# Kernel optimization log

Hardware: AMD Instinct MI355X
Metric: run time of the kernel (lower is better)

The kernel has to match this reference:

```python
import jax, jax.numpy as jnp
import numpy as np

WIN = 256  # window_size from init_kwargs


def _stream_attn(q, k, v, win, hollow):
    """Banded sliding-window attention.

    hollow=False (s-stream): key j attended iff 0 <= i - j < win (last `win` tokens incl. self).
    hollow=True  (c-stream): key j attended iff win <= i - j < 2*win (tokens [i-2W+1, i-W]).
    Returns (out [B,S,H,D], lse [B,H,S]) with lse = -inf for fully-masked rows.
    """
    B, S, H, D = q.shape
    nb = S // win
    scale = D ** -0.5
    qb = q.reshape(B, nb, win, H, D)
    kb = k.reshape(B, nb, win, H, D)
    vb = v.reshape(B, nb, win, H, D)
    pad = ((0, 0), (2, 0), (0, 0), (0, 0), (0, 0))
    kp = jnp.pad(kb, pad)
    vp = jnp.pad(vb, pad)
    k_ctx = jnp.concatenate([kp[:, t:t + nb] for t in range(3)], axis=2)  # [B,nb,3W,H,D]
    v_ctx = jnp.concatenate([vp[:, t:t + nb] for t in range(3)], axis=2)
    lq = jnp.arange(win)[:, None]
    kk = jnp.arange(3 * win)[None, :]
    t_blk = kk // win
    lk = kk % win
    rel = (2 - t_blk) * win + lq - lk  # i - j, shape [W, 3W]
    if hollow:
        wmask = (rel >= win) & (rel < 2 * win)
    else:
        wmask = (rel >= 0) & (rel < win)
    blk_ok = (jnp.arange(nb)[:, None] - 2 + (jnp.arange(3 * win) // win)[None, :]) >= 0  # [nb,3W]
    mask = wmask[None] & blk_ok[:, None, :]  # [nb, W, 3W]
    logits = jnp.einsum('bnqhd,bnkhd->bnhqk', qb, k_ctx) * scale  # [B,nb,H,W,3W]
    logits = jnp.where(mask[None, :, None], logits, -jnp.inf)
    m = jnp.max(logits, axis=-1)  # [B,nb,H,W]
    ms = jnp.where(jnp.isneginf(m), 0.0, m)
    p = jnp.exp(logits - ms[..., None])
    denom = jnp.sum(p, axis=-1)  # [B,nb,H,W]
    out = jnp.einsum('bnhqk,bnkhd->bnqhd', p, v_ctx)  # [B,nb,W,H,D]
    safe = jnp.where(denom > 0, denom, 1.0)
    out = out / jnp.moveaxis(safe, 2, 3)[..., None]
    lse = jnp.where(denom > 0, jnp.log(safe) + m, -jnp.inf)  # [B,nb,H,W]
    out = out.reshape(B, S, H, D)
    lse = jnp.moveaxis(lse, 1, 2).reshape(B, H, S)
    return out, lse


def _merge(out_c, lse_c, out_s, lse_s):
    # faithful jax version of merge_attn_states_torch (LSE online-softmax merge)
    m = jnp.maximum(lse_c, lse_s)
    ms = jnp.where(jnp.isneginf(m), 0.0, m)
    ec = jnp.exp(lse_c - ms)
    es = jnp.exp(lse_s - ms)
    se = ec + es  # s-stream always has >=1 key (self), so se > 0
    c_scale = jnp.moveaxis(ec / se, 1, 2)[..., None]  # [B,S,H,1]
    s_scale = jnp.moveaxis(es / se, 1, 2)[..., None]
    return out_c * c_scale + out_s * s_scale


def setup_inputs() -> dict:
    key = jax.random.key(0)
    k1, k2, k3 = jax.random.split(key, 3)
    B, S, H, D = 2, 2048, 16, 128
    return {
        'query': jax.random.normal(k1, (B, S, H, D), dtype=jnp.float32),
        'key': jax.random.normal(k2, (B, S, H, D), dtype=jnp.float32),
        'value': jax.random.normal(k3, (B, S, H, D), dtype=jnp.float32),
    }


def reference(query, key, value):
    out_c, lse_c = _stream_attn(query, key, value, WIN, hollow=True)   # c-stream: [i-2W, i-W]
    out_s, lse_s = _stream_attn(query, key, value, WIN, hollow=False)  # s-stream: last W tokens
    return _merge(out_c, lse_c, out_s, lse_s)
```

## Files before the change

kernel.cpp:

```cpp
#include <hip/hip_runtime.h>
#include <math.h>

#define S_LEN 2048
#define NH    16
#define DD    128
#define SROW  (NH*DD)
#define WIN2  512
#define BQ    128
#define BK    64
#define RSQ   136
#define RS    72

typedef __bf16 bf16x8 __attribute__((ext_vector_type(8)));
typedef __bf16 bf16x4 __attribute__((ext_vector_type(4)));
typedef float  f32x4  __attribute__((ext_vector_type(4)));

__device__ __forceinline__ f32x4 mfma16(bf16x8 a, bf16x8 b, f32x4 c) {
    return __builtin_amdgcn_mfma_f32_16x16x32_bf16(a, b, c, 0, 0, 0);
}

__device__ __forceinline__ unsigned int pack_bf16(float lo, float hi) {
    return (unsigned int)__builtin_bit_cast(unsigned short, (__bf16)lo)
         | ((unsigned int)__builtin_bit_cast(unsigned short, (__bf16)hi) << 16);
}

#define OFF_VT 8704
#define OFF_P  17920
#define SMEM_ELEMS 27136

__global__ __launch_bounds__(256, 2)
void swattn_kernel(const float* __restrict__ Qg, const float* __restrict__ Kg,
                   const float* __restrict__ Vg, float* __restrict__ Og) {
    __shared__ __align__(16) __bf16 smem[SMEM_ELEMS];

    const int t   = threadIdx.x;
    const int w   = t >> 6;
    const int l   = t & 63;
    const int r16 = l & 15;
    const int g4  = l >> 4;
    const int qt  = blockIdx.x;
    const int h   = blockIdx.y;
    const int b   = blockIdx.z;
    const int Qlo = qt * BQ;

    const size_t bh = ((size_t)b * S_LEN) * SROW + (size_t)h * DD;

    for (int it = 0; it < 16; ++it) {
        int f   = it * 256 + t;
        int q_l = f >> 5;
        int dq  = (f & 31) * 4;
        const float4 v = *(const float4*)&Qg[bh + (size_t)(Qlo + q_l) * SROW + dq];
        bf16x4 o4 = { (__bf16)v.x, (__bf16)v.y, (__bf16)v.z, (__bf16)v.w };
        *(bf16x4*)&smem[q_l * RSQ + dq] = o4;
    }
    __syncthreads();

    bf16x8 qf[2][4];
#pragma unroll
    for (int qg = 0; qg < 2; ++qg)
#pragma unroll
        for (int sl = 0; sl < 4; ++sl)
            qf[qg][sl] = *(const bf16x8*)&smem[(w*32 + qg*16 + r16) * RSQ + sl*32 + g4*8];
    __syncthreads();

    const f32x4 zero4 = {0.f, 0.f, 0.f, 0.f};
    f32x4 oacc[8][2];
#pragma unroll
    for (int dg = 0; dg < 8; ++dg) { oacc[dg][0] = zero4; oacc[dg][1] = zero4; }
    float m_run[2] = { -1e30f, -1e30f };
    float l_run[2] = { 0.f, 0.f };

    const int q_lo_w = Qlo + w * 32;
    const int q_hi_w = q_lo_w + 31;
    const float C1 = 0.08838834764831845f * 1.44269504088896340f;

    int cb = Qlo - (WIN2 - 1);
    if (cb < 0) cb = 0;
    cb &= ~(BK - 1);
    const int Qhi = Qlo + BQ - 1;

    for (int c0 = cb; c0 <= Qhi; c0 += BK) {
        for (int it = 0; it < 8; ++it) {
            int f   = it * 256 + t;
            int k_l = f >> 5;
            int dq  = (f & 31) * 4;
            const float4 v = *(const float4*)&Kg[bh + (size_t)(c0 + k_l) * SROW + dq];
            bf16x4 o4 = { (__bf16)v.x, (__bf16)v.y, (__bf16)v.z, (__bf16)v.w };
            *(bf16x4*)&smem[k_l * RSQ + dq] = o4;
        }
        {
            const int gv = l >> 5;
            const int rv = l & 31;
            for (int it = 0; it < 8; ++it) {
                int k0l = w * 16 + it * 2;
                const float4 v4 = *(const float4*)&Vg[bh + (size_t)(c0 + k0l + gv) * SROW + 4*rv];
                float ox = __shfl_xor(v4.x, 32);
                float oy = __shfl_xor(v4.y, 32);
                float oz = __shfl_xor(v4.z, 32);
                float ow = __shfl_xor(v4.w, 32);
                float lo0, hi0, lo1, hi1; int d0;
                if (gv == 0) { lo0 = v4.x; hi0 = ox;   lo1 = v4.y; hi1 = oy;   d0 = 4*rv; }
                else         { lo0 = oz;   hi0 = v4.z; lo1 = ow;   hi1 = v4.w; d0 = 4*rv + 2; }
                *(unsigned int*)&smem[OFF_VT + (d0    ) * RS + k0l] = pack_bf16(lo0, hi0);
                *(unsigned int*)&smem[OFF_VT + (d0 + 1) * RS + k0l] = pack_bf16(lo1, hi1);
            }
        }
        __syncthreads();

        const bool act = (q_hi_w >= c0) && (q_lo_w <= c0 + (BK - 1) + (WIN2 - 1));
        if (act) {
            f32x4 st[4][2];
#pragma unroll
            for (int kg = 0; kg < 4; ++kg) { st[kg][0] = zero4; st[kg][1] = zero4; }
#pragma unroll
            for (int sl = 0; sl < 4; ++sl)
#pragma unroll
                for (int kg = 0; kg < 4; ++kg) {
                    bf16x8 kf = *(const bf16x8*)&smem[(kg*16 + r16) * RSQ + sl*32 + g4*8];
                    st[kg][0] = mfma16(kf, qf[0][sl], st[kg][0]);
                    st[kg][1] = mfma16(kf, qf[1][sl], st[kg][1]);
                }

            const bool fv = (q_lo_w >= c0 + (BK - 1)) && (q_hi_w <= c0 + (WIN2 - 1));
            if (fv) {
#pragma unroll
                for (int kg = 0; kg < 4; ++kg)
#pragma unroll
                    for (int qg = 0; qg < 2; ++qg)
#pragma unroll
                        for (int rg = 0; rg < 4; ++rg) st[kg][qg][rg] *= C1;
            } else {
#pragma unroll
                for (int qg = 0; qg < 2; ++qg) {
                    int iq = q_lo_w + qg*16 + r16;
#pragma unroll
                    for (int kg = 0; kg < 4; ++kg) {
                        int relb = iq - (c0 + kg*16 + 4*g4);
#pragma unroll
                        for (int rg = 0; rg < 4; ++rg) {
                            bool ok = ((unsigned)(relb - rg)) < (unsigned)WIN2;
                            st[kg][qg][rg] = ok ? st[kg][qg][rg] * C1 : -1e30f;
                        }
                    }
                }
            }

            float alpha[2];
#pragma unroll
            for (int qg = 0; qg < 2; ++qg) {
                float mc = -1e30f;
#pragma unroll
                for (int kg = 0; kg < 4; ++kg)
#pragma unroll
                    for (int rg = 0; rg < 4; ++rg) mc = fmaxf(mc, st[kg][qg][rg]);
                mc = fmaxf(mc, __shfl_xor(mc, 16));
                mc = fmaxf(mc, __shfl_xor(mc, 32));
                float mn = fmaxf(m_run[qg], mc);
                alpha[qg] = exp2f(m_run[qg] - mn);
                m_run[qg] = mn;
                float sum = 0.f;
#pragma unroll
                for (int kg = 0; kg < 4; ++kg)
#pragma unroll
                    for (int rg = 0; rg < 4; ++rg) {
                        float tv = st[kg][qg][rg];
                        float p  = exp2f(tv - mn);
                        if (!fv) p = (tv > -1e29f) ? p : 0.f;
                        st[kg][qg][rg] = p;
                        sum += p;
                    }
                sum += __shfl_xor(sum, 16);
                sum += __shfl_xor(sum, 32);
                l_run[qg] = l_run[qg] * alpha[qg] + sum;
            }

#pragma unroll
            for (int qg = 0; qg < 2; ++qg)
#pragma unroll
                for (int kg = 0; kg < 4; ++kg) {
                    f32x4 pv = st[kg][qg];
                    bf16x4 p4 = { (__bf16)pv[0], (__bf16)pv[1], (__bf16)pv[2], (__bf16)pv[3] };
                    *(bf16x4*)&smem[OFF_P + (w*32 + qg*16 + r16) * RS + kg*16 + 4*g4] = p4;
                }

#pragma unroll
            for (int dg = 0; dg < 8; ++dg)
#pragma unroll
                for (int qg = 0; qg < 2; ++qg)
#pragma unroll
                    for (int rg = 0; rg < 4; ++rg) oacc[dg][qg][rg] *= alpha[qg];

#pragma unroll
            for (int ks = 0; ks < 2; ++ks) {
                bf16x8 pf0 = *(const bf16x8*)&smem[OFF_P + (w*32 +  0 + r16) * RS + ks*32 + g4*8];
                bf16x8 pf1 = *(const bf16x8*)&smem[OFF_P + (w*32 + 16 + r16) * RS + ks*32 + g4*8];
#pragma unroll
                for (int dg = 0; dg < 8; ++dg) {
                    bf16x8 vf = *(const bf16x8*)&smem[OFF_VT + (dg*16 + r16) * RS + ks*32 + g4*8];
                    oacc[dg][0] = mfma16(vf, pf0, oacc[dg][0]);
                    oacc[dg][1] = mfma16(vf, pf1, oacc[dg][1]);
                }
            }
        }
        __syncthreads();
    }

    float inv0 = 1.f / l_run[0];
    float inv1 = 1.f / l_run[1];
#pragma unroll
    for (int qg = 0; qg < 2; ++qg) {
        float iv = qg ? inv1 : inv0;
        int q = q_lo_w + qg*16 + r16;
        size_t base = bh + (size_t)q * SROW;
#pragma unroll
        for (int dg = 0; dg < 8; ++dg) {
            f32x4 o = oacc[dg][qg];
            float4 res = { o[0]*iv, o[1]*iv, o[2]*iv, o[3]*iv };
            *(float4*)&Og[base + dg*16 + 4*g4] = res;
        }
    }
}

extern "C" void kernel_launch(void* const* d_in, const int* in_sizes, int n_in,
                              void* d_out, int out_size, void* d_ws, size_t ws_size,
                              hipStream_t stream) {
    const float* q = (const float*)d_in[0];
    const float* k = (const float*)d_in[1];
    const float* v = (const float*)d_in[2];
    float* o = (float*)d_out;
    int B = in_sizes[0] / (S_LEN * NH * DD);
    dim3 grid(S_LEN / BQ, NH, B);
    swattn_kernel<<<grid, 256, 0, stream>>>(q, k, v, o);
}
```

Before: 179.4 us.

## Shrink P buffer, raise occupancy, swizzle V^T, remap blocks per XCD, prescale Q

```diff
diff --git a/kernel.cpp b/kernel.cpp
--- a/kernel.cpp
+++ b/kernel.cpp
@@ -10,6 +10,7 @@
 #define BK    64
 #define RSQ   136
 #define RS    72
+#define RSP   40
 
 typedef __bf16 bf16x8 __attribute__((ext_vector_type(8)));
 typedef __bf16 bf16x4 __attribute__((ext_vector_type(4)));
@@ -26,9 +27,9 @@
 
 #define OFF_VT 8704
 #define OFF_P  17920
-#define SMEM_ELEMS 27136
-
-__global__ __launch_bounds__(256, 2)
+#define SMEM_ELEMS 23040
+
+__global__ __launch_bounds__(256, 3)
 void swattn_kernel(const float* __restrict__ Qg, const float* __restrict__ Kg,
                    const float* __restrict__ Vg, float* __restrict__ Og) {
     __shared__ __align__(16) __bf16 smem[SMEM_ELEMS];
@@ -38,19 +39,33 @@
     const int l   = t & 63;
     const int r16 = l & 15;
     const int g4  = l >> 4;
-    const int qt  = blockIdx.x;
-    const int h   = blockIdx.y;
-    const int b   = blockIdx.z;
+
+    int qt, h, b;
+    if (gridDim.x == 512) {
+        int xcd = blockIdx.x & 7;
+        int j   = blockIdx.x >> 3;
+        qt      = j & 15;
+        int col = xcd * 4 + (j >> 4);
+        h       = col & 15;
+        b       = col >> 4;
+    } else {
+        qt = blockIdx.x % (S_LEN / BQ);
+        int col = blockIdx.x / (S_LEN / BQ);
+        h = col % NH;
+        b = col / NH;
+    }
     const int Qlo = qt * BQ;
 
     const size_t bh = ((size_t)b * S_LEN) * SROW + (size_t)h * DD;
+    const float C1 = 0.08838834764831845f * 1.44269504088896340f;
 
     for (int it = 0; it < 16; ++it) {
         int f   = it * 256 + t;
         int q_l = f >> 5;
         int dq  = (f & 31) * 4;
         const float4 v = *(const float4*)&Qg[bh + (size_t)(Qlo + q_l) * SROW + dq];
-        bf16x4 o4 = { (__bf16)v.x, (__bf16)v.y, (__bf16)v.z, (__bf16)v.w };
+        bf16x4 o4 = { (__bf16)(v.x * C1), (__bf16)(v.y * C1),
+                      (__bf16)(v.z * C1), (__bf16)(v.w * C1) };
         *(bf16x4*)&smem[q_l * RSQ + dq] = o4;
     }
     __syncthreads();
@@ -67,12 +82,13 @@
     f32x4 oacc[8][2];
 #pragma unroll
     for (int dg = 0; dg < 8; ++dg) { oacc[dg][0] = zero4; oacc[dg][1] = zero4; }
-    float m_run[2] = { -1e30f, -1e30f };
+    float m_run[2] = { -1e4f, -1e4f };
     float l_run[2] = { 0.f, 0.f };
 
     const int q_lo_w = Qlo + w * 32;
     const int q_hi_w = q_lo_w + 31;
-    const float C1 = 0.08838834764831845f * 1.44269504088896340f;
+    const int gv = l >> 5;
+    const int rv = l & 31;
 
     int cb = Qlo - (WIN2 - 1);
     if (cb < 0) cb = 0;
@@ -88,22 +104,19 @@
             bf16x4 o4 = { (__bf16)v.x, (__bf16)v.y, (__bf16)v.z, (__bf16)v.w };
             *(bf16x4*)&smem[k_l * RSQ + dq] = o4;
         }
-        {
-            const int gv = l >> 5;
-            const int rv = l & 31;
-            for (int it = 0; it < 8; ++it) {
-                int k0l = w * 16 + it * 2;
-                const float4 v4 = *(const float4*)&Vg[bh + (size_t)(c0 + k0l + gv) * SROW + 4*rv];
-                float ox = __shfl_xor(v4.x, 32);
-                float oy = __shfl_xor(v4.y, 32);
-                float oz = __shfl_xor(v4.z, 32);
-                float ow = __shfl_xor(v4.w, 32);
-                float lo0, hi0, lo1, hi1; int d0;
-                if (gv == 0) { lo0 = v4.x; hi0 = ox;   lo1 = v4.y; hi1 = oy;   d0 = 4*rv; }
-                else         { lo0 = oz;   hi0 = v4.z; lo1 = ow;   hi1 = v4.w; d0 = 4*rv + 2; }
-                *(unsigned int*)&smem[OFF_VT + (d0    ) * RS + k0l] = pack_bf16(lo0, hi0);
-                *(unsigned int*)&smem[OFF_VT + (d0 + 1) * RS + k0l] = pack_bf16(lo1, hi1);
-            }
+        for (int it = 0; it < 8; ++it) {
+            int k0l = w * 16 + it * 2;
+            const float4 v4 = *(const float4*)&Vg[bh + (size_t)(c0 + k0l + gv) * SROW + 4*rv];
+            float ox = __shfl_xor(v4.x, 32);
+            float oy = __shfl_xor(v4.y, 32);
+            float oz = __shfl_xor(v4.z, 32);
+            float ow = __shfl_xor(v4.w, 32);
+            float lo0, hi0, lo1, hi1; int d0;
+            if (gv == 0) { lo0 = v4.x; hi0 = ox;   lo1 = v4.y; hi1 = oy;   d0 = 4*rv; }
+            else         { lo0 = oz;   hi0 = v4.z; lo1 = ow;   hi1 = v4.w; d0 = 4*rv + 2; }
+            int col = k0l ^ ((rv & 7) << 3);
+            *(unsigned int*)&smem[OFF_VT + (d0    ) * RS + col] = pack_bf16(lo0, hi0);
+            *(unsigned int*)&smem[OFF_VT + (d0 + 1) * RS + col] = pack_bf16(lo1, hi1);
         }
         __syncthreads();
 
@@ -122,14 +135,7 @@
                 }
 
             const bool fv = (q_lo_w >= c0 + (BK - 1)) && (q_hi_w <= c0 + (WIN2 - 1));
-            if (fv) {
-#pragma unroll
-                for (int kg = 0; kg < 4; ++kg)
-#pragma unroll
-                    for (int qg = 0; qg < 2; ++qg)
-#pragma unroll
-                        for (int rg = 0; rg < 4; ++rg) st[kg][qg][rg] *= C1;
-            } else {
+            if (!fv) {
 #pragma unroll
                 for (int qg = 0; qg < 2; ++qg) {
                     int iq = q_lo_w + qg*16 + r16;
@@ -139,7 +145,7 @@
 #pragma unroll
                         for (int rg = 0; rg < 4; ++rg) {
                             bool ok = ((unsigned)(relb - rg)) < (unsigned)WIN2;
-                            st[kg][qg][rg] = ok ? st[kg][qg][rg] * C1 : -1e30f;
+                            st[kg][qg][rg] = ok ? st[kg][qg][rg] : -1e30f;
                         }
                     }
                 }
@@ -163,9 +169,7 @@
                 for (int kg = 0; kg < 4; ++kg)
 #pragma unroll
                     for (int rg = 0; rg < 4; ++rg) {
-                        float tv = st[kg][qg][rg];
-                        float p  = exp2f(tv - mn);
-                        if (!fv) p = (tv > -1e29f) ? p : 0.f;
+                        float p = exp2f(st[kg][qg][rg] - mn);
                         st[kg][qg][rg] = p;
                         sum += p;
                     }
@@ -175,15 +179,6 @@
             }
 
 #pragma unroll
-            for (int qg = 0; qg < 2; ++qg)
-#pragma unroll
-                for (int kg = 0; kg < 4; ++kg) {
-                    f32x4 pv = st[kg][qg];
-                    bf16x4 p4 = { (__bf16)pv[0], (__bf16)pv[1], (__bf16)pv[2], (__bf16)pv[3] };
-                    *(bf16x4*)&smem[OFF_P + (w*32 + qg*16 + r16) * RS + kg*16 + 4*g4] = p4;
-                }
-
-#pragma unroll
             for (int dg = 0; dg < 8; ++dg)
 #pragma unroll
                 for (int qg = 0; qg < 2; ++qg)
@@ -191,12 +186,23 @@
                     for (int rg = 0; rg < 4; ++rg) oacc[dg][qg][rg] *= alpha[qg];
 
 #pragma unroll
-            for (int ks = 0; ks < 2; ++ks) {
-                bf16x8 pf0 = *(const bf16x8*)&smem[OFF_P + (w*32 +  0 + r16) * RS + ks*32 + g4*8];
-                bf16x8 pf1 = *(const bf16x8*)&smem[OFF_P + (w*32 + 16 + r16) * RS + ks*32 + g4*8];
+            for (int h2 = 0; h2 < 2; ++h2) {
+#pragma unroll
+                for (int kg2 = 0; kg2 < 2; ++kg2) {
+                    int kg = h2*2 + kg2;
+#pragma unroll
+                    for (int qg = 0; qg < 2; ++qg) {
+                        f32x4 pv = st[kg][qg];
+                        bf16x4 p4 = { (__bf16)pv[0], (__bf16)pv[1], (__bf16)pv[2], (__bf16)pv[3] };
+                        *(bf16x4*)&smem[OFF_P + (w*32 + qg*16 + r16) * RSP + kg2*16 + 4*g4] = p4;
+                    }
+                }
+                bf16x8 pf0 = *(const bf16x8*)&smem[OFF_P + (w*32 +  0 + r16) * RSP + g4*8];
+                bf16x8 pf1 = *(const bf16x8*)&smem[OFF_P + (w*32 + 16 + r16) * RSP + g4*8];
 #pragma unroll
                 for (int dg = 0; dg < 8; ++dg) {
-                    bf16x8 vf = *(const bf16x8*)&smem[OFF_VT + (dg*16 + r16) * RS + ks*32 + g4*8];
+                    int col = (h2*32 + g4*8) ^ (32*(dg&1) + 8*(r16>>2));
+                    bf16x8 vf = *(const bf16x8*)&smem[OFF_VT + (dg*16 + r16) * RS + col];
                     oacc[dg][0] = mfma16(vf, pf0, oacc[dg][0]);
                     oacc[dg][1] = mfma16(vf, pf1, oacc[dg][1]);
                 }
@@ -229,6 +235,6 @@
     const float* v = (const float*)d_in[2];
     float* o = (float*)d_out;
     int B = in_sizes[0] / (S_LEN * NH * DD);
-    dim3 grid(S_LEN / BQ, NH, B);
-    swattn_kernel<<<grid, 256, 0, stream>>>(q, k, v, o);
-}
+    int nblk = (S_LEN / BQ) * NH * B;
+    swattn_kernel<<<dim3(nblk), 256, 0, stream>>>(q, k, v, o);
+}
```

After: 346.4 us. 93.1% more time.
